# Optimization experiments

Hardware: AMD Instinct MI355X
Metric: run time of the kernel (lower is better)

Reference implementation:

```python
import jax, jax.numpy as jnp
import numpy as np

BS, N, K, S = 512, 500, 100, 96  # batch, nodes per sample, kriged nodes per sample, seq_len
HID, AUG = 32, 2
TAU = 0.1


def setup_inputs() -> dict:
    key = jax.random.key(0)
    ks = jax.random.split(key, 8)
    x = jax.random.normal(ks[0], (BS * N, S), jnp.float32)
    y = jax.random.normal(ks[1], (BS * N, S), jnp.float32)
    W1 = jax.random.normal(ks[2], (S, HID), jnp.float32) / np.sqrt(S)
    b1 = jnp.zeros((HID,), jnp.float32)
    W2 = jax.random.normal(ks[3], (HID, AUG), jnp.float32) / np.sqrt(HID)
    b2 = jnp.zeros((AUG,), jnp.float32)
    # unique node indices per sample (torch index-assign with dups is ill-defined)
    perm_keys = jax.random.split(ks[4], BS)
    krig_idx = jax.vmap(lambda k: jax.random.permutation(k, N)[:K])(perm_keys).astype(jnp.int32)
    idx_of_node = jnp.full((BS,), N, jnp.int32)  # nodes per sample
    mask = (jax.random.uniform(ks[5], (BS * K, S)) > 0.1).astype(jnp.float32)
    gumbel = jax.random.gumbel(ks[6], (BS * K, AUG), jnp.float32)
    return {"x": x, "y": y, "W1": W1, "b1": b1, "W2": W2, "b2": b2,
            "mask": mask, "gumbel": gumbel, "krig_idx": krig_idx,
            "idx_of_node": idx_of_node}


def reference(x, y, W1, b1, W2, b2, mask, gumbel, krig_idx, idx_of_node):
    bs, k = krig_idx.shape
    num_nodes = x.shape[0] // bs
    s = x.shape[1]
    # gather kriged node series: [bs, num_nodes, S] -> [bs*K, S]
    y3 = y.reshape(bs, num_nodes, s)
    smp = jnp.take_along_axis(y3, krig_idx[:, :, None], axis=1).reshape(bs * k, s)
    # tiny MLP on gathered features (krig_feat == smp, same gather done twice in torch)
    h = jax.nn.relu(smp @ W1 + b1)
    logits = h @ W2 + b2
    # hard gumbel-softmax, straight-through
    y_soft = jax.nn.softmax((logits + gumbel) / TAU, axis=-1)
    y_hard = jax.nn.one_hot(jnp.argmax(y_soft, axis=-1), logits.shape[-1], dtype=y_soft.dtype)
    gb = y_hard - jax.lax.stop_gradient(y_soft) + y_soft  # [bs*K, 2]
    # data_aug = [zeros, mask*smp] (detached); sum over aug dim == gb[:,1]*masked
    val = gb[:, 1:2] * jax.lax.stop_gradient(mask * smp)  # [bs*K, S]
    # flat row indices: per-sample offsets from shifted cumsum of idx_of_node
    offs = jnp.cumsum(jnp.concatenate([jnp.zeros((1,), idx_of_node.dtype), idx_of_node])[:-1])
    flat = (offs[:, None] + krig_idx).reshape(-1)  # [bs*K]
    return x.at[flat].set(val)
```

## Files before the change

kernel.cpp:

```cpp
#include <hip/hip_runtime.h>

#define BSZ 512
#define NN  500
#define KK  100
#define SS  96
#define HIDN 32
#define ROWS (BSZ * NN)
#define NF4  (ROWS * SS / 4)
#define F4PR (SS / 4)
#define NSLOT 8
#define FUSE_BLOCKS (NF4 / (256 * NSLOT))

typedef float vf4 __attribute__((ext_vector_type(4)));


__global__ __launch_bounds__(512) void prep_kernel(const int* __restrict__ idx_of_node,
                                                   int* __restrict__ offs,
                                                   int4* __restrict__ flag2_4) {
    if (blockIdx.x == 0) {
        __shared__ int buf[BSZ];
        int t = threadIdx.x;
        int v = idx_of_node[t];
        buf[t] = v;
        __syncthreads();
        int acc = v;
        for (int d = 1; d < BSZ; d <<= 1) {
            int add = (t >= d) ? buf[t - d] : 0;
            __syncthreads();
            acc += add;
            buf[t] = acc;
            __syncthreads();
        }
        offs[t] = acc - v;
    }
    int n4 = ROWS / 2;
    for (int i = blockIdx.x * 512 + threadIdx.x; i < n4; i += gridDim.x * 512)
        flag2_4[i] = make_int4(-1, 0, -1, 0);
}

__global__ __launch_bounds__(256) void gate_kernel(
    const float* __restrict__ y, const float* __restrict__ W1,
    const float* __restrict__ b1, const float* __restrict__ W2,
    const float* __restrict__ b2, const float* __restrict__ gumbel,
    const int* __restrict__ krig_idx, const int* __restrict__ offs,
    int2* __restrict__ flag2) {
    __shared__ float4 w1s[SS * HIDN / 4];
    __shared__ float b1s[HIDN];
    __shared__ float w2s[HIDN * 2];
    __shared__ float b2s[2];
    for (int i = threadIdx.x; i < SS * HIDN / 4; i += 256)
        w1s[i] = reinterpret_cast<const float4*>(W1)[i];
    if (threadIdx.x < HIDN) b1s[threadIdx.x] = b1[threadIdx.x];
    if (threadIdx.x < 2 * HIDN) w2s[threadIdx.x] = W2[threadIdx.x];
    if (threadIdx.x < 2) b2s[threadIdx.x] = b2[threadIdx.x];
    __syncthreads();

    int r = blockIdx.x * 256 + threadIdx.x;
    if (r >= BSZ * KK) return;
    int b = r / KK;
    int node = krig_idx[r];
    const float4* yrow = reinterpret_cast<const float4*>(y + (size_t)(b * NN + node) * SS);

    float h[HIDN];
#pragma unroll
    for (int j = 0; j < HIDN; ++j) h[j] = b1s[j];
#pragma unroll
    for (int s4 = 0; s4 < F4PR; ++s4) {
        float4 v = yrow[s4];
        float vv[4] = {v.x, v.y, v.z, v.w};
        const float4* wbase = &w1s[s4 * 4 * (HIDN / 4)];
#pragma unroll
        for (int q = 0; q < 4; ++q) {
#pragma unroll
            for (int j4 = 0; j4 < HIDN / 4; ++j4) {
                float4 w = wbase[q * (HIDN / 4) + j4];
                h[j4 * 4 + 0] += vv[q] * w.x;
                h[j4 * 4 + 1] += vv[q] * w.y;
                h[j4 * 4 + 2] += vv[q] * w.z;
                h[j4 * 4 + 3] += vv[q] * w.w;
            }
        }
    }
    float l0 = b2s[0], l1 = b2s[1];
#pragma unroll
    for (int j = 0; j < HIDN; ++j) {
        float hr = fmaxf(h[j], 0.0f);
        l0 += hr * w2s[j * 2 + 0];
        l1 += hr * w2s[j * 2 + 1];
    }
    float g0 = gumbel[r * 2 + 0], g1 = gumbel[r * 2 + 1];
    int on = (l1 + g1 > l0 + g0);
    flag2[offs[b] + node] = make_int2(on ? (b * NN + node) : -2, r);
}

__global__ __launch_bounds__(256) void fuse_kernel(
    const vf4* __restrict__ x4, const vf4* __restrict__ y4,
    const vf4* __restrict__ mask4, const int2* __restrict__ flag2,
    vf4* __restrict__ out4) {
    const int t0 = blockIdx.x * (256 * NSLOT) + threadIdx.x;

    int2 fg[NSLOT];
#pragma unroll
    for (int k = 0; k < NSLOT; ++k) {
        int idx = t0 + k * 256;
        fg[k] = flag2[idx / F4PR];
    }
    vf4 xv[NSLOT];
#pragma unroll
    for (int k = 0; k < NSLOT; ++k) {
        int idx = t0 + k * 256;
        int code = fg[k].x;
        vf4 v = (vf4)(0.0f);
        if (code == -1) {
            v = x4[idx];
        } else if (code >= 0) {
            int row = idx / F4PR;
            int c = idx - row * F4PR;
            vf4 m = mask4[fg[k].y * F4PR + c];
            v = m * y4[code * F4PR + c];
        }
        xv[k] = v;
    }
#pragma unroll
    for (int k = 0; k < NSLOT; ++k) {
        int idx = t0 + k * 256;
        __builtin_nontemporal_store(xv[k], out4 + idx);
    }
}

extern "C" void kernel_launch(void* const* d_in, const int* in_sizes, int n_in,
                              void* d_out, int out_size, void* d_ws, size_t ws_size,
                              hipStream_t stream) {
    const float* x      = (const float*)d_in[0];
    const float* y      = (const float*)d_in[1];
    const float* W1     = (const float*)d_in[2];
    const float* b1     = (const float*)d_in[3];
    const float* W2     = (const float*)d_in[4];
    const float* b2     = (const float*)d_in[5];
    const float* mask   = (const float*)d_in[6];
    const float* gumbel = (const float*)d_in[7];
    const int* krig_idx = (const int*)d_in[8];
    const int* idx_of_node = (const int*)d_in[9];
    float* out = (float*)d_out;

    int* offs = (int*)d_ws;
    int2* flag2 = (int2*)(offs + BSZ);

    prep_kernel<<<128, 512, 0, stream>>>(idx_of_node, offs,
                                         reinterpret_cast<int4*>(flag2));

    int rows = BSZ * KK;
    gate_kernel<<<(rows + 255) / 256, 256, 0, stream>>>(
        y, W1, b1, W2, b2, gumbel, krig_idx, offs, flag2);

    fuse_kernel<<<FUSE_BLOCKS, 256, 0, stream>>>(
        reinterpret_cast<const vf4*>(x), reinterpret_cast<const vf4*>(y),
        reinterpret_cast<const vf4*>(mask), flag2,
        reinterpret_cast<vf4*>(out));
}
```

Baseline: 59.53 us.

## Shrink per-row flag to a single int and move nontemporal hint to x loads

The per-row flag array becomes one int holding the kriged row index r (or -1/-2) instead of an int2 pair, which halves the flag traffic written by prep and read by fuse. The fuse kernel now recovers the source y row by reading krig_idx[r], adding a dependent load on the kriged path. The nontemporal hint moves from the output stores to the x loads, so out is written with normal stores. Overall the change trades a smaller flag buffer for an extra indirection and different cache behaviour.

Result: slower. 64.36 us (+8.1%).

```diff
diff --git a/kernel.cpp b/kernel.cpp
--- a/kernel.cpp
+++ b/kernel.cpp
@@ -16,7 +16,7 @@
 
 __global__ __launch_bounds__(512) void prep_kernel(const int* __restrict__ idx_of_node,
                                                    int* __restrict__ offs,
-                                                   int4* __restrict__ flag2_4) {
+                                                   int4* __restrict__ flag4) {
     if (blockIdx.x == 0) {
         __shared__ int buf[BSZ];
         int t = threadIdx.x;
@@ -33,9 +33,9 @@
         }
         offs[t] = acc - v;
     }
-    int n4 = ROWS / 2;
+    int n4 = ROWS / 4;
     for (int i = blockIdx.x * 512 + threadIdx.x; i < n4; i += gridDim.x * 512)
-        flag2_4[i] = make_int4(-1, 0, -1, 0);
+        flag4[i] = make_int4(-1, -1, -1, -1);
 }
 
 __global__ __launch_bounds__(256) void gate_kernel(
@@ -43,7 +43,7 @@
     const float* __restrict__ b1, const float* __restrict__ W2,
     const float* __restrict__ b2, const float* __restrict__ gumbel,
     const int* __restrict__ krig_idx, const int* __restrict__ offs,
-    int2* __restrict__ flag2) {
+    int* __restrict__ flag) {
     __shared__ float4 w1s[SS * HIDN / 4];
     __shared__ float b1s[HIDN];
     __shared__ float w2s[HIDN * 2];
@@ -90,41 +90,43 @@
     }
     float g0 = gumbel[r * 2 + 0], g1 = gumbel[r * 2 + 1];
     int on = (l1 + g1 > l0 + g0);
-    flag2[offs[b] + node] = make_int2(on ? (b * NN + node) : -2, r);
+    flag[offs[b] + node] = on ? r : -2;
 }
 
 __global__ __launch_bounds__(256) void fuse_kernel(
     const vf4* __restrict__ x4, const vf4* __restrict__ y4,
-    const vf4* __restrict__ mask4, const int2* __restrict__ flag2,
-    vf4* __restrict__ out4) {
+    const vf4* __restrict__ mask4, const int* __restrict__ flag,
+    const int* __restrict__ krig_idx, vf4* __restrict__ out4) {
     const int t0 = blockIdx.x * (256 * NSLOT) + threadIdx.x;
 
-    int2 fg[NSLOT];
+    int fr[NSLOT];
 #pragma unroll
     for (int k = 0; k < NSLOT; ++k) {
         int idx = t0 + k * 256;
-        fg[k] = flag2[idx / F4PR];
+        fr[k] = flag[idx / F4PR];
     }
     vf4 xv[NSLOT];
 #pragma unroll
     for (int k = 0; k < NSLOT; ++k) {
         int idx = t0 + k * 256;
-        int code = fg[k].x;
+        int r = fr[k];
         vf4 v = (vf4)(0.0f);
-        if (code == -1) {
-            v = x4[idx];
-        } else if (code >= 0) {
+        if (r == -1) {
+            v = __builtin_nontemporal_load(x4 + idx);
+        } else if (r >= 0) {
             int row = idx / F4PR;
             int c = idx - row * F4PR;
-            vf4 m = mask4[fg[k].y * F4PR + c];
-            v = m * y4[code * F4PR + c];
+            int b = r / KK;
+            int node = krig_idx[r];
+            vf4 m = mask4[r * F4PR + c];
+            v = m * y4[(b * NN + node) * F4PR + c];
         }
         xv[k] = v;
     }
 #pragma unroll
     for (int k = 0; k < NSLOT; ++k) {
         int idx = t0 + k * 256;
-        __builtin_nontemporal_store(xv[k], out4 + idx);
+        out4[idx] = xv[k];
     }
 }
 
@@ -144,17 +146,17 @@
     float* out = (float*)d_out;
 
     int* offs = (int*)d_ws;
-    int2* flag2 = (int2*)(offs + BSZ);
+    int* flag = offs + BSZ;
 
     prep_kernel<<<128, 512, 0, stream>>>(idx_of_node, offs,
-                                         reinterpret_cast<int4*>(flag2));
+                                         reinterpret_cast<int4*>(flag));
 
     int rows = BSZ * KK;
     gate_kernel<<<(rows + 255) / 256, 256, 0, stream>>>(
-        y, W1, b1, W2, b2, gumbel, krig_idx, offs, flag2);
+        y, W1, b1, W2, b2, gumbel, krig_idx, offs, flag);
 
     fuse_kernel<<<FUSE_BLOCKS, 256, 0, stream>>>(
         reinterpret_cast<const vf4*>(x), reinterpret_cast<const vf4*>(y),
-        reinterpret_cast<const vf4*>(mask), flag2,
+        reinterpret_cast<const vf4*>(mask), flag, krig_idx,
         reinterpret_cast<vf4*>(out));
 }
```
